# Optimization experiments

Hardware: AMD Instinct MI355X
Metric: run time of the kernel (lower is better)

## Reference

```python
import jax, jax.numpy as jnp
import numpy as np

T, B, E, F = 2048, 8, 512, 2
N = E * F  # state dim = emb_dim * exp_factor


def setup_inputs() -> dict:
    key = jax.random.key(0)
    ks = jax.random.split(key, 14)
    x = jax.random.normal(ks[0], (T, B, E), dtype=jnp.float32)
    # in/out projections (torch Linear: y = x @ W.T + b; we store W already transposed)
    W_in = jax.random.normal(ks[1], (E, N), dtype=jnp.float32) / np.sqrt(E)
    b_in = jnp.zeros((N,), dtype=jnp.float32)
    W_out = jax.random.normal(ks[2], (N, E), dtype=jnp.float32) / np.sqrt(N)
    b_out = jnp.zeros((E,), dtype=jnp.float32)
    # LRU eigenvalue parameterization (r_min=0, r_max=1)
    u1 = jax.random.uniform(ks[3], (N,), dtype=jnp.float32, minval=1e-4, maxval=1.0)
    u2 = jax.random.uniform(ks[4], (N,), dtype=jnp.float32)
    nu_log = jnp.log(-0.5 * jnp.log(u1))
    theta_log = jnp.log(u2 * 2.0 * np.pi)
    gamma_log = jnp.log(jnp.sqrt(1.0 - jnp.exp(-jnp.exp(nu_log)) ** 2))
    B_real = jax.random.normal(ks[5], (N, N), dtype=jnp.float32) / np.sqrt(2 * E)
    B_imag = jax.random.normal(ks[6], (N, N), dtype=jnp.float32) / np.sqrt(2 * N)
    C_real = jax.random.normal(ks[7], (N, N), dtype=jnp.float32) / np.sqrt(N)
    C_imag = jax.random.normal(ks[8], (N, N), dtype=jnp.float32) / np.sqrt(N)
    D = jax.random.normal(ks[9], (N,), dtype=jnp.float32)
    return {"x": x, "W_in": W_in, "b_in": b_in, "W_out": W_out, "b_out": b_out,
            "nu_log": nu_log, "theta_log": theta_log, "gamma_log": gamma_log,
            "B_real": B_real, "B_imag": B_imag, "C_real": C_real, "C_imag": C_imag,
            "D": D}


def _bin_op(el1, el2):
    a_i, bu_i = el1
    a_j, bu_j = el2
    return (a_j * a_i, a_j * bu_i + bu_j)


def reference(x, W_in, b_in, W_out, b_out, nu_log, theta_log, gamma_log,
              B_real, B_imag, C_real, C_imag, D):
    u = x @ W_in + b_in                                   # [T,B,N] real
    Lam = jnp.exp(-jnp.exp(nu_log) + 1j * jnp.exp(theta_log))        # [N] complex
    B_norm = (B_real + 1j * B_imag) * jnp.exp(gamma_log)[:, None]    # [N,N]
    C = C_real + 1j * C_imag                                          # [N,N]
    # Bu[t,b,j] = sum_i B_norm[i,j] * u[t,b,i]  (matches einsum 'ij,kmi->kmj')
    Bu = jnp.einsum('ij,tbi->tbj', B_norm, u.astype(B_norm.dtype))   # [T,B,N]
    Lam_elems = jnp.broadcast_to(Lam, Bu.shape)                       # [T,B,N]
    # linear recurrence h_t = Lam * h_{t-1} + Bu_t via associative scan over time (axis 0)
    _, h = jax.lax.associative_scan(_bin_op, (Lam_elems, Bu), axis=0)
    y = (jnp.einsum('ij,tbi->tbj', C, h) + D * u).real                # [T,B,N]
    return y @ W_out + b_out                                          # [T,B,E]
```

## Files before the change

### kernel.cpp

```cpp
#include <hip/hip_runtime.h>
#include <hip/hip_bf16.h>

typedef __hip_bfloat16 bf16;
typedef __attribute__((ext_vector_type(8))) short bf16x8;
typedef __attribute__((ext_vector_type(4))) float f32x4;

#define T_DIM 2048
#define B_DIM 8
#define E_DIM 512
#define N_DIM 1024
#define M_ROWS (T_DIM * B_DIM)
#define NCHUNK 64
#define CLEN (T_DIM / NCHUNK)

__device__ __forceinline__ void gload16(const void* g, void* l) {
    __builtin_amdgcn_global_load_lds((const void __attribute__((address_space(1)))*)g,
                                     (void __attribute__((address_space(3)))*)l, 16, 0, 0);
}

__global__ void k_prep(const float* __restrict__ nu_log, const float* __restrict__ theta_log,
                       const float* __restrict__ gamma_log,
                       float* __restrict__ LamR, float* __restrict__ LamI, float* __restrict__ g) {
    int i = blockIdx.x * 256 + threadIdx.x;
    if (i < N_DIM) {
        float nu  = expf(nu_log[i]);
        float th  = expf(theta_log[i]);
        float mag = expf(-nu);
        LamR[i] = mag * cosf(th);
        LamI[i] = mag * sinf(th);
        g[i] = expf(gamma_log[i]);
    }
}

struct __align__(8) bf4 { bf16 v[4]; };
__global__ void k_conv(const float* __restrict__ in, bf16* __restrict__ out, int n4, float mul) {
    int i = blockIdx.x * 256 + threadIdx.x;
    int stride = gridDim.x * 256;
    for (; i < n4; i += stride) {
        float4 v = ((const float4*)in)[i];
        bf4 o;
        o.v[0] = __float2bfloat16(v.x * mul);
        o.v[1] = __float2bfloat16(v.y * mul);
        o.v[2] = __float2bfloat16(v.z * mul);
        o.v[3] = __float2bfloat16(v.w * mul);
        ((bf4*)out)[i] = o;
    }
}

__global__ void k_transpose(const float* __restrict__ in, bf16* __restrict__ out,
                            const float* __restrict__ scale, int R, int C) {
    __shared__ float tile[32][33];
    int tx = threadIdx.x & 31, ty = threadIdx.x >> 5;
    int r0 = blockIdx.y * 32, c0 = blockIdx.x * 32;
#pragma unroll
    for (int i = 0; i < 32; i += 8) {
        int r = r0 + ty + i;
        float v = in[(size_t)r * C + c0 + tx];
        if (scale) v *= scale[r];
        tile[ty + i][tx] = v;
    }
    __syncthreads();
#pragma unroll
    for (int i = 0; i < 32; i += 8) {
        out[(size_t)(c0 + ty + i) * R + r0 + tx] = __float2bfloat16(tile[tx][ty + i]);
    }
}

__global__ void k_bias_bu(const float* __restrict__ b_in, const float* __restrict__ g,
                          const float* __restrict__ B_real, const float* __restrict__ B_imag,
                          float* __restrict__ c_bu) {
    int id = blockIdx.x;
    int jblk = id & 7, ic = id >> 3;
    int j = jblk * 256 + threadIdx.x;
    const float* B = (j < N_DIM) ? B_real : B_imag;
    int jj = j & (N_DIM - 1);
    float s = 0.f;
    for (int i = ic * 128; i < ic * 128 + 128; ++i)
        s = fmaf(b_in[i] * g[i], B[(size_t)i * N_DIM + jj], s);
    atomicAdd(&c_bu[j], s);
}

__global__ void k_bias_out(const float* __restrict__ b_out, const float* __restrict__ b_in,
                           const float* __restrict__ D, const float* __restrict__ W_out,
                           float* __restrict__ bo) {
    int id = blockIdx.x;
    int eblk = id & 1, ic = id >> 1;
    int e = eblk * 256 + threadIdx.x;
    float s = (ic == 0) ? b_out[e] : 0.f;
    for (int j = ic * 128; j < ic * 128 + 128; ++j)
        s = fmaf(b_in[j] * D[j], W_out[(size_t)j * E_DIM + e], s);
    atomicAdd(&bo[e], s);
}

template <bool BIAS>
__device__ __forceinline__ void gemm128_core(bf16* lA, bf16* lB,
        const bf16* __restrict__ A, int lda, const bf16* __restrict__ Bt, int ldb,
        bf16* __restrict__ outp, int ldo, const float* __restrict__ bias, int K,
        int bn, int bm) {
    const int tid = threadIdx.x;
    const int lane = tid & 63, w = tid >> 6;
    const int wr = w >> 1, wc = w & 1;
    const int fr = lane & 15, fq = lane >> 4;
    f32x4 acc[4][4] = {};
    for (int k0 = 0; k0 < K; k0 += 32) {
#pragma unroll
        for (int L = 0; L < 2; ++L) {
            int idx = L * 256 + tid;
            int rr = idx >> 2, kk = (idx & 3) * 8;
            gload16(A + (size_t)(bm * 128 + rr) * lda + k0 + kk, lA + idx * 8);
            gload16(Bt + (size_t)(bn * 128 + rr) * ldb + k0 + kk, lB + idx * 8);
        }
        __syncthreads();
        bf16x8 af[4], bfr[4];
#pragma unroll
        for (int i = 0; i < 4; ++i)
            af[i] = *(const bf16x8*)(lA + (wr * 64 + i * 16 + fr) * 32 + fq * 8);
#pragma unroll
        for (int i = 0; i < 4; ++i)
            bfr[i] = *(const bf16x8*)(lB + (wc * 64 + i * 16 + fr) * 32 + fq * 8);
#pragma unroll
        for (int i = 0; i < 4; ++i)
#pragma unroll
            for (int j = 0; j < 4; ++j)
                acc[i][j] = __builtin_amdgcn_mfma_f32_16x16x32_bf16(af[i], bfr[j], acc[i][j], 0, 0, 0);
        __syncthreads();
    }
    const int orow = bm * 128 + wr * 64;
    const int ocol = bn * 128 + wc * 64;
#pragma unroll
    for (int i = 0; i < 4; ++i)
#pragma unroll
        for (int j = 0; j < 4; ++j) {
            int col = ocol + j * 16 + fr;
            float bv = BIAS ? bias[col] : 0.0f;
#pragma unroll
            for (int r = 0; r < 4; ++r) {
                int row = orow + i * 16 + fq * 4 + r;
                outp[(size_t)row * ldo + col] = __float2bfloat16(acc[i][j][r] + bv);
            }
        }
}

__global__ __launch_bounds__(256)
void k_g1(const bf16* __restrict__ xb, const bf16* __restrict__ WBcat,
          bf16* __restrict__ BuH, const float* __restrict__ c_bu) {
    __shared__ __align__(16) bf16 lA[128 * 32];
    __shared__ __align__(16) bf16 lB[128 * 32];
    int id = blockIdx.x;
    int swz = (id & 7) * 256 + (id >> 3);
    int bn = swz & 15, bm = swz >> 4;
    gemm128_core<true>(lA, lB, xb, 512, WBcat, 512, BuH, 2048, c_bu, 512, bn, bm);
}

__global__ __launch_bounds__(256)
void k_gemm4(const bf16* __restrict__ BscT, const bf16* __restrict__ Win_b,
             const bf16* __restrict__ WoT, const bf16* __restrict__ WoTD,
             const bf16* __restrict__ Cr_b, const bf16* __restrict__ Ci_b,
             bf16* __restrict__ WBcat, bf16* __restrict__ Bfin) {
    __shared__ __align__(16) bf16 lA[128 * 32];
    __shared__ __align__(16) bf16 lB[128 * 32];
    int id = blockIdx.x;
    if (id < 64) {
        gemm128_core<false>(lA, lB, BscT, 1024, Win_b, 1024, WBcat, 512, nullptr, 1024, id & 3, id >> 2);
    } else if (id < 96) {
        int l = id - 64;
        gemm128_core<false>(lA, lB, WoT, 1024, Cr_b, 1024, Bfin, 2560, nullptr, 1024, l & 7, l >> 3);
    } else if (id < 128) {
        int l = id - 96;
        gemm128_core<false>(lA, lB, WoT, 1024, Ci_b, 1024, Bfin + 1024, 2560, nullptr, 1024, l & 7, l >> 3);
    } else {
        int l = id - 128;
        gemm128_core<false>(lA, lB, WoTD, 1024, Win_b, 1024, Bfin + 2048, 2560, nullptr, 1024, l & 3, l >> 2);
    }
}

template <bool ASPLIT>
__global__ __launch_bounds__(256, 1)
void k_gemm_wn(const bf16* __restrict__ A0, const bf16* __restrict__ A1, int ksplit,
               int lda0, int lda1, const bf16* __restrict__ Bt, int ldb,
               float* __restrict__ outp, int ldo, const float* __restrict__ bias, int K) {
    __shared__ __align__(16) bf16 lA[2][64 * 32];
    __shared__ __align__(16) bf16 lB[2][512 * 32];
    const int tid = threadIdx.x;
    const int bm = blockIdx.x;
    const int lane = tid & 63, w = tid >> 6;
    const int fr = lane & 15, fq = lane >> 4;
    f32x4 acc[4][8] = {};
    const int nt = K / 32;

    auto stage = [&](int buf, int t) {
        int k0 = t * 32;
        const bf16* Ap = A0; int lda = lda0, ac = k0;
        if (ASPLIT && k0 >= ksplit) { Ap = A1; lda = lda1; ac = k0 - ksplit; }
        {
            int rr = tid >> 2, s = tid & 3;
            int kk = (s ^ (rr & 3)) * 8;
            gload16(Ap + (size_t)(bm * 64 + rr) * lda + ac + kk, &lA[buf][tid * 8]);
        }
#pragma unroll
        for (int L = 0; L < 8; ++L) {
            int idx = L * 256 + tid;
            int rr = idx >> 2, s = idx & 3;
            int kk = (s ^ (rr & 3)) * 8;
            gload16(Bt + (size_t)rr * ldb + k0 + kk, &lB[buf][idx * 8]);
        }
    };

    stage(0, 0);
    __syncthreads();
    int cur = 0;
    for (int t = 0; t < nt; ++t) {
        if (t + 1 < nt) stage(cur ^ 1, t + 1);
        bf16x8 af[4], bfr[8];
#pragma unroll
        for (int i = 0; i < 4; ++i) {
            int rr = i * 16 + fr;
            af[i] = *(const bf16x8*)(&lA[cur][(rr * 4 + (fq ^ (rr & 3))) * 8]);
        }
#pragma unroll
        for (int j = 0; j < 8; ++j) {
            int rr = w * 128 + j * 16 + fr;
            bfr[j] = *(const bf16x8*)(&lB[cur][(rr * 4 + (fq ^ (rr & 3))) * 8]);
        }
#pragma unroll
        for (int i = 0; i < 4; ++i)
#pragma unroll
            for (int j = 0; j < 8; ++j)
                acc[i][j] = __builtin_amdgcn_mfma_f32_16x16x32_bf16(af[i], bfr[j], acc[i][j], 0, 0, 0);
        __syncthreads();
        cur ^= 1;
    }
    const int orow = bm * 64;
#pragma unroll
    for (int i = 0; i < 4; ++i)
#pragma unroll
        for (int j = 0; j < 8; ++j) {
            int col = w * 128 + j * 16 + fr;
            float bv = bias[col];
#pragma unroll
            for (int r = 0; r < 4; ++r)
                outp[(size_t)(orow + i * 16 + fq * 4 + r) * ldo + col] = acc[i][j][r] + bv;
        }
}

__global__ void k_scan_carry(const bf16* __restrict__ BuH, const float* __restrict__ LamR,
                             const float* __restrict__ LamI, float2* __restrict__ carry) {
    int tid = blockIdx.x * 256 + threadIdx.x;
    int n = tid & (N_DIM - 1);
    int bb = (tid >> 10) & 7;
    int c = tid >> 13;
    float lr = LamR[n], li = LamI[n];
    float hr = 0.f, hi = 0.f;
    const bf16* p = BuH + ((size_t)(c * CLEN) * B_DIM + bb) * 2048 + n;
#pragma unroll 8
    for (int t = 0; t < CLEN; ++t) {
        float br = __bfloat162float(p[0]);
        float bi = __bfloat162float(p[N_DIM]);
        float nr = fmaf(lr, hr, fmaf(-li, hi, br));
        float ni = fmaf(lr, hi, fmaf(li, hr, bi));
        hr = nr; hi = ni;
        p += B_DIM * 2048;
    }
    carry[tid] = make_float2(hr, hi);
}

__global__ void k_scan_combine(const float2* __restrict__ carry, float2* __restrict__ S,
                               const float* __restrict__ LamR, const float* __restrict__ LamI) {
    int tid = blockIdx.x * 256 + threadIdx.x;
    int n = tid & (N_DIM - 1);
    float ar = LamR[n], ai = LamI[n];
#pragma unroll
    for (int s = 0; s < 5; ++s) { float nr = ar * ar - ai * ai, ni = 2.f * ar * ai; ar = nr; ai = ni; }
    float sr = 0.f, si = 0.f;
    for (int c = 0; c < NCHUNK; ++c) {
        S[(size_t)c * 8192 + tid] = make_float2(sr, si);
        float2 ca = carry[(size_t)c * 8192 + tid];
        float nr = fmaf(ar, sr, fmaf(-ai, si, ca.x));
        float ni = fmaf(ar, si, fmaf(ai, sr, ca.y));
        sr = nr; si = ni;
    }
}

__global__ void k_scan_apply(bf16* __restrict__ BuH, const float* __restrict__ LamR,
                             const float* __restrict__ LamI, const float2* __restrict__ S) {
    int tid = blockIdx.x * 256 + threadIdx.x;
    int n = tid & (N_DIM - 1);
    int bb = (tid >> 10) & 7;
    int c = tid >> 13;
    float lr = LamR[n], li = LamI[n];
    float2 s0 = S[tid];
    float hr = s0.x, hi = s0.y;
    bf16* p = BuH + ((size_t)(c * CLEN) * B_DIM + bb) * 2048 + n;
#pragma unroll 8
    for (int t = 0; t < CLEN; ++t) {
        float br = __bfloat162float(p[0]);
        float bi = __bfloat162float(p[N_DIM]);
        float nr = fmaf(lr, hr, fmaf(-li, hi, br));
        float ni = fmaf(lr, hi, fmaf(li, hr, bi));
        hr = nr; hi = ni;
        p[0] = __float2bfloat16(hr);
        p[N_DIM] = __float2bfloat16(hi);
        p += B_DIM * 2048;
    }
}

extern "C" void kernel_launch(void* const* d_in, const int* in_sizes, int n_in,
                              void* d_out, int out_size, void* d_ws, size_t ws_size,
                              hipStream_t stream) {
    const float* x         = (const float*)d_in[0];
    const float* W_in      = (const float*)d_in[1];
    const float* b_in      = (const float*)d_in[2];
    const float* W_out     = (const float*)d_in[3];
    const float* b_out     = (const float*)d_in[4];
    const float* nu_log    = (const float*)d_in[5];
    const float* theta_log = (const float*)d_in[6];
    const float* gamma_log = (const float*)d_in[7];
    const float* B_real    = (const float*)d_in[8];
    const float* B_imag    = (const float*)d_in[9];
    const float* C_real    = (const float*)d_in[10];
    const float* C_imag    = (const float*)d_in[11];
    const float* Dvec      = (const float*)d_in[12];
    float* out = (float*)d_out;

    char* ws = (char*)d_ws;
    size_t off = 0;
    auto alloc = [&](size_t bytes) { void* p = ws + off; off = (off + bytes + 255) & ~(size_t)255; return p; };
    bf16*  xb    = (bf16*)alloc((size_t)M_ROWS * E_DIM * 2);
    bf16*  BuH   = (bf16*)alloc((size_t)M_ROWS * 2048 * 2);
    bf16*  BscT  = (bf16*)alloc((size_t)2048 * 1024 * 2);
    bf16*  Win_b = (bf16*)alloc((size_t)512 * 1024 * 2);
    bf16*  Cr_b  = (bf16*)alloc((size_t)1024 * 1024 * 2);
    bf16*  Ci_b  = (bf16*)alloc((size_t)1024 * 1024 * 2);
    bf16*  WoT   = (bf16*)alloc((size_t)512 * 1024 * 2);
    bf16*  WoTD  = (bf16*)alloc((size_t)512 * 1024 * 2);
    bf16*  WBcat = (bf16*)alloc((size_t)2048 * 512 * 2);
    bf16*  Bfin  = (bf16*)alloc((size_t)512 * 2560 * 2);
    float* LamR  = (float*)alloc(1024 * 4);
    float* LamI  = (float*)alloc(1024 * 4);
    float* gvec  = (float*)alloc(1024 * 4);
    float* c_bu  = (float*)alloc(2048 * 4);
    float* biasO = (float*)alloc(512 * 4);
    float2* carry = (float2*)alloc((size_t)NCHUNK * 8192 * 8);
    float2* Sbuf  = (float2*)alloc((size_t)NCHUNK * 8192 * 8);

    k_prep<<<4, 256, 0, stream>>>(nu_log, theta_log, gamma_log, LamR, LamI, gvec);
    k_conv<<<2048, 256, 0, stream>>>(x, xb, M_ROWS * E_DIM / 4, 1.f);
    k_conv<<<512, 256, 0, stream>>>(W_in, Win_b, 512 * 1024 / 4, 1.f);
    k_conv<<<1024, 256, 0, stream>>>(C_real, Cr_b, 1024 * 1024 / 4, 1.f);
    k_conv<<<1024, 256, 0, stream>>>(C_imag, Ci_b, 1024 * 1024 / 4, -1.f);
    k_transpose<<<dim3(32, 32), 256, 0, stream>>>(B_real, BscT, gvec, 1024, 1024);
    k_transpose<<<dim3(32, 32), 256, 0, stream>>>(B_imag, BscT + (size_t)1024 * 1024, gvec, 1024, 1024);
    k_transpose<<<dim3(16, 32), 256, 0, stream>>>(W_out, WoT, nullptr, 1024, 512);
    k_transpose<<<dim3(16, 32), 256, 0, stream>>>(W_out, WoTD, Dvec, 1024, 512);

    hipMemsetAsync(c_bu, 0, 2048 * 4, stream);
    hipMemsetAsync(biasO, 0, 512 * 4, stream);
    k_bias_bu<<<64, 256, 0, stream>>>(b_in, gvec, B_real, B_imag, c_bu);
    k_bias_out<<<16, 256, 0, stream>>>(b_out, b_in, Dvec, W_out, biasO);

    k_gemm4<<<144, 256, 0, stream>>>(BscT, Win_b, WoT, WoTD, Cr_b, Ci_b, WBcat, Bfin);

    k_g1<<<2048, 256, 0, stream>>>(xb, WBcat, BuH, c_bu);

    k_scan_carry<<<NCHUNK * 8192 / 256, 256, 0, stream>>>(BuH, LamR, LamI, carry);
    k_scan_combine<<<32, 256, 0, stream>>>(carry, Sbuf, LamR, LamI);
    k_scan_apply<<<NCHUNK * 8192 / 256, 256, 0, stream>>>(BuH, LamR, LamI, Sbuf);

    k_gemm_wn<true><<<256, 256, 0, stream>>>(BuH, xb, 2048, 2048, 512, Bfin, 2560, out, 512, biasO, 2560);
}
```

Measured before the change: 412.4 us.

## Retile final GEMM to 128x256 blocks with 8 waves and swizzled block order

The final output GEMM moves from 64x512 tiles with 4 waves and double-buffered LDS to 128x256 tiles with 8 waves (2x4 warp grid, 64x64 per wave), a single LDS buffer and two barriers per k-step. Block indices are swizzled so neighbouring blocks share A/B panels, aiming at better L2 reuse and occupancy. The single buffer means the next stage's loads wait until the current fragments are read, which may expose more load latency than the previous double-buffered scheme.

Measured after the change: 378.4 us. 8.2% less time.

```diff
diff --git a/kernel.cpp b/kernel.cpp
--- a/kernel.cpp
+++ b/kernel.cpp
@@ -175,67 +175,69 @@
 }
 
 template <bool ASPLIT>
-__global__ __launch_bounds__(256, 1)
-void k_gemm_wn(const bf16* __restrict__ A0, const bf16* __restrict__ A1, int ksplit,
+__global__ __launch_bounds__(512)
+void k_gemm_db(const bf16* __restrict__ A0, const bf16* __restrict__ A1, int ksplit,
                int lda0, int lda1, const bf16* __restrict__ Bt, int ldb,
                float* __restrict__ outp, int ldo, const float* __restrict__ bias, int K) {
-    __shared__ __align__(16) bf16 lA[2][64 * 32];
-    __shared__ __align__(16) bf16 lB[2][512 * 32];
+    __shared__ __align__(16) bf16 lA[128 * 32];
+    __shared__ __align__(16) bf16 lB[256 * 32];
     const int tid = threadIdx.x;
-    const int bm = blockIdx.x;
+    int id = blockIdx.x;
+    int swz = (id & 7) * 32 + (id >> 3);
+    const int bm = swz >> 1, bn = swz & 1;
     const int lane = tid & 63, w = tid >> 6;
+    const int wr = w >> 2, wc = w & 3;
     const int fr = lane & 15, fq = lane >> 4;
-    f32x4 acc[4][8] = {};
+    f32x4 acc[4][4] = {};
     const int nt = K / 32;
 
-    auto stage = [&](int buf, int t) {
+    auto stage = [&](int t) {
         int k0 = t * 32;
         const bf16* Ap = A0; int lda = lda0, ac = k0;
         if (ASPLIT && k0 >= ksplit) { Ap = A1; lda = lda1; ac = k0 - ksplit; }
         {
             int rr = tid >> 2, s = tid & 3;
             int kk = (s ^ (rr & 3)) * 8;
-            gload16(Ap + (size_t)(bm * 64 + rr) * lda + ac + kk, &lA[buf][tid * 8]);
-        }
-#pragma unroll
-        for (int L = 0; L < 8; ++L) {
-            int idx = L * 256 + tid;
+            gload16(Ap + (size_t)(bm * 128 + rr) * lda + ac + kk, lA + tid * 8);
+        }
+#pragma unroll
+        for (int L = 0; L < 2; ++L) {
+            int idx = L * 512 + tid;
             int rr = idx >> 2, s = idx & 3;
             int kk = (s ^ (rr & 3)) * 8;
-            gload16(Bt + (size_t)rr * ldb + k0 + kk, &lB[buf][idx * 8]);
+            gload16(Bt + (size_t)(bn * 256 + rr) * ldb + k0 + kk, lB + idx * 8);
         }
     };
 
-    stage(0, 0);
-    __syncthreads();
-    int cur = 0;
+    stage(0);
     for (int t = 0; t < nt; ++t) {
-        if (t + 1 < nt) stage(cur ^ 1, t + 1);
-        bf16x8 af[4], bfr[8];
+        __syncthreads();
+        bf16x8 af[4], bfr[4];
 #pragma unroll
         for (int i = 0; i < 4; ++i) {
-            int rr = i * 16 + fr;
-            af[i] = *(const bf16x8*)(&lA[cur][(rr * 4 + (fq ^ (rr & 3))) * 8]);
-        }
-#pragma unroll
-        for (int j = 0; j < 8; ++j) {
-            int rr = w * 128 + j * 16 + fr;
-            bfr[j] = *(const bf16x8*)(&lB[cur][(rr * 4 + (fq ^ (rr & 3))) * 8]);
-        }
+            int rr = wr * 64 + i * 16 + fr;
+            af[i] = *(const bf16x8*)(lA + (rr * 4 + (fq ^ (rr & 3))) * 8);
+        }
+#pragma unroll
+        for (int j = 0; j < 4; ++j) {
+            int rr = wc * 64 + j * 16 + fr;
+            bfr[j] = *(const bf16x8*)(lB + (rr * 4 + (fq ^ (rr & 3))) * 8);
+        }
+        __syncthreads();
+        if (t + 1 < nt) stage(t + 1);
 #pragma unroll
         for (int i = 0; i < 4; ++i)
 #pragma unroll
-            for (int j = 0; j < 8; ++j)
+            for (int j = 0; j < 4; ++j)
                 acc[i][j] = __builtin_amdgcn_mfma_f32_16x16x32_bf16(af[i], bfr[j], acc[i][j], 0, 0, 0);
-        __syncthreads();
-        cur ^= 1;
-    }
-    const int orow = bm * 64;
+    }
+    const int orow = bm * 128 + wr * 64;
+    const int ocol = bn * 256 + wc * 64;
 #pragma unroll
     for (int i = 0; i < 4; ++i)
 #pragma unroll
-        for (int j = 0; j < 8; ++j) {
-            int col = w * 128 + j * 16 + fr;
+        for (int j = 0; j < 4; ++j) {
+            int col = ocol + j * 16 + fr;
             float bv = bias[col];
 #pragma unroll
             for (int r = 0; r < 4; ++r)
@@ -366,5 +368,5 @@
     k_scan_combine<<<32, 256, 0, stream>>>(carry, Sbuf, LamR, LamI);
     k_scan_apply<<<NCHUNK * 8192 / 256, 256, 0, stream>>>(BuH, LamR, LamI, Sbuf);
 
-    k_gemm_wn<true><<<256, 256, 0, stream>>>(BuH, xb, 2048, 2048, 512, Bfin, 2560, out, 512, biasO, 2560);
-}
+    k_gemm_db<true><<<256, 512, 0, stream>>>(BuH, xb, 2048, 2048, 512, Bfin, 2560, out, 512, biasO, 2560);
+}
```
